# Performance work log

Measured on AMD Instinct MI355X. Metric: run time of the kernel, lower is better.

Reference implementation:

```python
import jax, jax.numpy as jnp
import numpy as np

N_ATOMS = 100000
N_BONDS = 200000
N_MOLS = 4000
ATOMS_PER_MOL = 25
MAX_NB = 6
ATOM_FDIM = 133
BOND_FDIM = 14
HIDDEN = 300
DEPTH = 3


def setup_inputs() -> dict:
    key = jax.random.key(0)
    ks = jax.random.split(key, 8)
    f_atoms = jax.random.normal(ks[0], (N_ATOMS, ATOM_FDIM), dtype=jnp.float32)
    f_bonds = jax.random.normal(ks[1], (N_BONDS, BOND_FDIM), dtype=jnp.float32)
    # incoming-bond lists per atom (irregular gather targets)
    a2b = jax.random.randint(ks[2], (N_ATOMS, MAX_NB), 0, N_BONDS, dtype=jnp.int32)
    # source atom of each directed bond
    b2a = jax.random.randint(ks[3], (N_BONDS,), 0, N_ATOMS, dtype=jnp.int32)
    # reverse bond: directed bonds come in pairs (2i, 2i+1)
    b2revb = (jnp.arange(N_BONDS, dtype=jnp.int32) ^ 1)
    # contiguous [start, size] per molecule
    starts = jnp.arange(N_MOLS, dtype=jnp.int32) * ATOMS_PER_MOL
    sizes = jnp.full((N_MOLS,), ATOMS_PER_MOL, dtype=jnp.int32)
    a_scope = jnp.stack([starts, sizes], axis=1)
    W_i = jax.random.normal(ks[4], (HIDDEN, ATOM_FDIM + BOND_FDIM), dtype=jnp.float32) * 0.05
    W_h = jax.random.normal(ks[5], (HIDDEN, HIDDEN), dtype=jnp.float32) * 0.05
    W_o = jax.random.normal(ks[6], (HIDDEN, ATOM_FDIM + HIDDEN), dtype=jnp.float32) * 0.05
    b_o = jax.random.normal(ks[7], (HIDDEN,), dtype=jnp.float32) * 0.05
    return {"f_atoms": f_atoms, "f_bonds": f_bonds, "a2b": a2b, "b2a": b2a,
            "b2revb": b2revb, "a_scope": a_scope, "W_i": W_i, "W_h": W_h,
            "W_o": W_o, "b_o": b_o}


def reference(f_atoms, f_bonds, a2b, b2a, b2revb, a_scope, W_i, W_h, W_o, b_o):
    # initial directed-bond messages: [f_atoms[src], f_bonds] -> Linear -> ReLU
    input_feats = jnp.concatenate([f_atoms[b2a], f_bonds], axis=1)  # (E, 147)
    message = jax.nn.relu(input_feats @ W_i.T)  # (E, H)
    for _ in range(DEPTH - 1):
        nei_a_message = message[a2b].sum(axis=1)          # (V, H) gather+sum
        nei_message = nei_a_message[b2a] - message[b2revb]  # (E, H)
        message = jax.nn.relu(nei_message @ W_h.T)
    a_message = message[a2b].sum(axis=1)  # (V, H)
    atom_hiddens = jax.nn.relu(jnp.concatenate([f_atoms, a_message], axis=1) @ W_o.T + b_o)
    # vectorized scope mean-pool (scopes are contiguous ranges)
    starts = a_scope[:, 0]
    sizes = a_scope[:, 1]
    seg_ids = jnp.searchsorted(starts, jnp.arange(atom_hiddens.shape[0]), side='right') - 1
    sums = jax.ops.segment_sum(atom_hiddens, seg_ids, num_segments=N_MOLS)
    denom = jnp.maximum(sizes, 1).astype(atom_hiddens.dtype)[:, None]
    mol_vecs = jnp.where((sizes > 0)[:, None], sums / denom, 0.0)
    return mol_vecs
```

## Files before the change

kernel.cpp:

```cpp
#include <hip/hip_runtime.h>
#include <stdint.h>

#define N_ATOMS   100000
#define N_BONDS   200000
#define N_MOLS    4000
#define MAX_NB    6
#define ATOM_FDIM 133
#define BOND_FDIM 14
#define HIDDEN    300
#define NPAD      320

typedef __attribute__((ext_vector_type(8))) short          bf16x8;
typedef __attribute__((ext_vector_type(8))) unsigned short u16x8;
typedef __attribute__((ext_vector_type(4))) float          f32x4;
typedef __attribute__((ext_vector_type(4))) unsigned int   u32x4;

static __device__ __forceinline__ float u2f(unsigned int u) {
  union { unsigned int u; float f; } v; v.u = u; return v.f;
}
static __device__ __forceinline__ unsigned int f2u(float f) {
  union { float f; unsigned int u; } v; v.f = f; return v.u;
}
static __device__ __forceinline__ float bflo(unsigned int u) { return u2f(u << 16); }
static __device__ __forceinline__ float bfhi(unsigned int u) { return u2f(u & 0xffff0000u); }
static __device__ __forceinline__ unsigned short f2bf_rn(float f) {
  unsigned int u = f2u(f);
  return (unsigned short)((u + 0x7fffu + ((u >> 16) & 1u)) >> 16);
}
static __device__ __forceinline__ unsigned int pack_rn(float lo, float hi) {
  return ((unsigned int)f2bf_rn(hi) << 16) | f2bf_rn(lo);
}

__global__ __launch_bounds__(256) void convin_kernel(
    const float* __restrict__ w, unsigned short* __restrict__ o, int N, int K, int KP) {
  size_t total = (size_t)N * KP;
  for (size_t idx = (size_t)blockIdx.x * 256 + threadIdx.x; idx < total; idx += (size_t)gridDim.x * 256) {
    int n = (int)(idx / KP), k = (int)(idx - (size_t)n * KP);
    float v = (k < K) ? w[(size_t)n * K + k] : 0.f;
    o[idx] = f2bf_rn(v);
  }
}

__global__ __launch_bounds__(256) void convw_kernel(
    const float* __restrict__ w, unsigned short* __restrict__ o,
    int Ksrc, int seg1, int src2off, int seg2dst, int seg2len, int KP) {
  int total = NPAD * KP;
  for (int idx = blockIdx.x * 256 + threadIdx.x; idx < total; idx += gridDim.x * 256) {
    int n = idx / KP, k = idx - n * KP;
    int src = -1;
    if (k < seg1) src = k;
    else if (k >= seg2dst && k < seg2dst + seg2len) src = src2off + (k - seg2dst);
    float v = (n < HIDDEN && src >= 0) ? w[(size_t)n * Ksrc + src] : 0.f;
    o[idx] = f2bf_rn(v);
  }
}

template<int KP, int SEG, bool RELU>
__global__ __launch_bounds__(256) void gemm_tp(
    const unsigned short* S1, const unsigned short* __restrict__ S2,
    const int* __restrict__ gmap, const unsigned short* __restrict__ W,
    unsigned short* out, int M, int nTiles) {
  constexpr int CHUNKS = KP / 8;
  constexpr int NST    = KP / 32;
  __shared__ __align__(16) unsigned short As[2 * 64 * KP];

  const int tid  = threadIdx.x;
  const int lane = tid & 63;
  const int wv   = tid >> 6;
  const int ar   = lane & 15, kq = lane >> 4;
  const int nbase = wv * 80;
  const unsigned short* Wl = W + (size_t)(nbase + ar) * KP + kq * 8;

  auto rowof = [&](int tile) { int r = tile * 64 + lane; return (r < M) ? r : (M - 1); };

  auto stage = [&](int buf, int drow, int srow) {
    char* base = (char*)As + (size_t)buf * (64 * KP * 2);
#pragma unroll
    for (int cs = wv; cs < CHUNKS; cs += 4) {
      const unsigned short* src;
      if (SEG == 0) src = S1 + (size_t)drow * KP + cs * 8;
      else src = (cs < 20) ? (S1 + (size_t)srow * 160 + cs * 8)
                           : (S2 + (size_t)drow * 32 + (cs - 20) * 8);
      __builtin_amdgcn_global_load_lds(
          (const __attribute__((address_space(1))) void*)src,
          (__attribute__((address_space(3))) void*)(base + (size_t)cs * 1024), 16, 0, 0);
    }
  };

  f32x4 acc[4][5];

  auto compute = [&](int buf) {
    const char* base = (const char*)As + (size_t)buf * (64 * KP * 2);
    bf16x8 bnxt[5];
#pragma unroll
    for (int nf = 0; nf < 5; nf++) bnxt[nf] = *(const bf16x8*)(Wl + (size_t)nf * 16 * KP);
#pragma unroll
    for (int ks = 0; ks < NST; ks++) {
      bf16x8 bcur[5];
#pragma unroll
      for (int nf = 0; nf < 5; nf++) bcur[nf] = bnxt[nf];
      if (ks + 1 < NST) {
#pragma unroll
        for (int nf = 0; nf < 5; nf++)
          bnxt[nf] = *(const bf16x8*)(Wl + (size_t)nf * 16 * KP + (ks + 1) * 32);
      }
      bf16x8 af[4];
#pragma unroll
      for (int m = 0; m < 4; m++)
        af[m] = *(const bf16x8*)(base + (size_t)((ks * 4 + kq) * 64 + m * 16 + ar) * 16);
#pragma unroll
      for (int nf = 0; nf < 5; nf++)
#pragma unroll
        for (int m = 0; m < 4; m++)
          acc[m][nf] = __builtin_amdgcn_mfma_f32_16x16x32_bf16(af[m], bcur[nf], acc[m][nf], 0, 0, 0);
    }
  };

  auto storeC = [&](int tile) {
#pragma unroll
    for (int m = 0; m < 4; m++)
#pragma unroll
      for (int rr = 0; rr < 4; rr++) {
        int orow = tile * 64 + m * 16 + kq * 4 + rr;
        if (orow >= M) continue;
#pragma unroll
        for (int nf = 0; nf < 5; nf++) {
          float v = acc[m][nf][rr];
          if (RELU) v = v > 0.f ? v : 0.f;
          out[(size_t)orow * NPAD + nbase + nf * 16 + ar] = f2bf_rn(v);
        }
      }
  };

  int t = blockIdx.x;
  if (t >= nTiles) return;
  {
    int srow0 = (SEG == 1) ? gmap[rowof(t)] : 0;
    stage(0, rowof(t), srow0);
  }
  int tn = t + gridDim.x;
  int g_n = (SEG == 1 && tn < nTiles) ? gmap[rowof(tn)] : 0;
  __syncthreads();

  int cur = 0;
  while (t < nTiles) {
    const int nxt = t + gridDim.x;
    if (nxt < nTiles) stage(cur ^ 1, rowof(nxt), g_n);
    const int t2 = nxt + gridDim.x;
    int g_n2 = (SEG == 1 && t2 < nTiles) ? gmap[rowof(t2)] : 0;
#pragma unroll
    for (int m = 0; m < 4; m++)
#pragma unroll
      for (int n = 0; n < 5; n++) acc[m][n] = (f32x4){0.f, 0.f, 0.f, 0.f};
    compute(cur);
    __syncthreads();
    storeC(t);
    cur ^= 1; t = nxt; g_n = g_n2;
  }
}

__global__ __launch_bounds__(256) void gemm_tpf(
    const unsigned short* Z, const unsigned short* __restrict__ Nei,
    const int* __restrict__ b2a, const unsigned short* __restrict__ W,
    unsigned short* out, int nTiles) {
  constexpr int KP = 320, BK = 160, NCH = 2, NSTC = 5, NREG = 5;
  __shared__ __align__(16) unsigned short As[2 * 64 * BK];

  const int tid  = threadIdx.x;
  const int lane = tid & 63;
  const int wv   = tid >> 6;
  const int ar   = lane & 15, kq = lane >> 4;
  const int nbase = wv * 80;
  const unsigned short* Wl = W + (size_t)(nbase + ar) * KP + kq * 8;

  u32x4 nei4[NREG], z4[NREG];

  auto loadreg = [&](int tile, int chunk) {
    const int row = tile * 64 + lane;
    const int g   = b2a[row];
    const int rev = row ^ 1;
    const int kb  = chunk * BK;
#pragma unroll
    for (int i = 0; i < NREG; i++) {
      const int cs = i * 4 + wv;
      nei4[i] = *(const u32x4*)(Nei + (size_t)g * NPAD + kb + cs * 8);
      z4[i]   = *(const u32x4*)(Z + (size_t)rev * NPAD + kb + cs * 8);
    }
  };

  auto writestage = [&](int buf) {
    char* base = (char*)As + (size_t)buf * (64 * BK * 2);
#pragma unroll
    for (int i = 0; i < NREG; i++) {
      const int cs = i * 4 + wv;
      u32x4 o;
#pragma unroll
      for (int t4 = 0; t4 < 4; t4++) {
        float lo = bflo(nei4[i][t4]) - bflo(z4[i][t4]);
        float hi = bfhi(nei4[i][t4]) - bfhi(z4[i][t4]);
        lo = lo > 0.f ? lo : 0.f; hi = hi > 0.f ? hi : 0.f;
        o[t4] = pack_rn(lo, hi);
      }
      *(u32x4*)(base + (size_t)(cs * 64 + lane) * 16) = o;
    }
  };

  f32x4 acc[4][5];

  auto compute = [&](int buf, int chunk) {
    const char* base = (const char*)As + (size_t)buf * (64 * BK * 2);
    const int kb = chunk * BK;
#pragma unroll
    for (int ks = 0; ks < NSTC; ks++) {
      bf16x8 af[4];
#pragma unroll
      for (int m = 0; m < 4; m++)
        af[m] = *(const bf16x8*)(base + (size_t)((ks * 4 + kq) * 64 + m * 16 + ar) * 16);
#pragma unroll
      for (int nf = 0; nf < 5; nf++) {
        bf16x8 bfr = *(const bf16x8*)(Wl + (size_t)nf * 16 * KP + kb + ks * 32);
#pragma unroll
        for (int m = 0; m < 4; m++)
          acc[m][nf] = __builtin_amdgcn_mfma_f32_16x16x32_bf16(af[m], bfr, acc[m][nf], 0, 0, 0);
      }
    }
  };

  auto storeC = [&](int tile) {
#pragma unroll
    for (int m = 0; m < 4; m++)
#pragma unroll
      for (int rr = 0; rr < 4; rr++) {
        int orow = tile * 64 + m * 16 + kq * 4 + rr;
#pragma unroll
        for (int nf = 0; nf < 5; nf++)
          out[(size_t)orow * NPAD + nbase + nf * 16 + ar] = f2bf_rn(acc[m][nf][rr]);
      }
  };

  int t = blockIdx.x;
  if (t >= nTiles) return;
  loadreg(t, 0);
  writestage(0);
  __syncthreads();

  int cur = 0;
  while (t < nTiles) {
#pragma unroll
    for (int m = 0; m < 4; m++)
#pragma unroll
      for (int n = 0; n < 5; n++) acc[m][n] = (f32x4){0.f, 0.f, 0.f, 0.f};
#pragma unroll
    for (int c = 0; c < NCH; c++) {
      int nt = t, nc = c + 1;
      if (nc == NCH) { nt = t + gridDim.x; nc = 0; }
      const bool valid = nt < nTiles;
      if (valid) loadreg(nt, nc);
      compute(cur, c);
      if (valid) writestage(cur ^ 1);
      __syncthreads();
      cur ^= 1;
    }
    storeC(t);
    t += gridDim.x;
  }
}

__global__ __launch_bounds__(256, 2) void gemm_bpo(
    const float* __restrict__ Af, const unsigned short* Ab,
    const unsigned short* __restrict__ W, const float* __restrict__ bias,
    unsigned short* out, int M) {
  constexpr int KP = 480, NST = 15;
  __shared__ __align__(16) unsigned short As[NST * 2048];

  const int b0   = blockIdx.x * 64;
  const int tid  = threadIdx.x;
  const int lane = tid & 63;
  const int wave = tid >> 6;
  const int sr   = tid >> 2;
  const int q    = tid & 3;

  int row = b0 + sr;
  if (row >= M) row = M - 1;
  const int dbase = (sr >> 4) * 512 + (q * 16 + (sr & 15)) * 8;

  auto stage_chunk = [&](int ks) -> u16x8 {
    const int kc = ks * 32 + q * 8;
    u16x8 r;
    if (kc >= 160) {
      r = *(const u16x8*)(Ab + (size_t)row * NPAD + (kc - 160));
    } else {
#pragma unroll
      for (int j = 0; j < 8; j++) {
        int k = kc + j;
        r[j] = (k < ATOM_FDIM) ? f2bf_rn(Af[(size_t)row * ATOM_FDIM + k]) : (unsigned short)0;
      }
    }
    return r;
  };

  constexpr int G = 5;
#pragma unroll
  for (int ks0 = 0; ks0 < NST; ks0 += G) {
    u16x8 vals[G];
#pragma unroll
    for (int j = 0; j < G; j++) { int ks = ks0 + j; if (ks < NST) vals[j] = stage_chunk(ks); }
#pragma unroll
    for (int j = 0; j < G; j++) { int ks = ks0 + j; if (ks < NST) *(u16x8*)&As[ks * 2048 + dbase] = vals[j]; }
  }
  __syncthreads();

  f32x4 acc[4][5];
#pragma unroll
  for (int m = 0; m < 4; m++)
#pragma unroll
    for (int n = 0; n < 5; n++) acc[m][n] = (f32x4){0.f, 0.f, 0.f, 0.f};

  const int nbase = wave * 80;
  const int ar = lane & 15, kq = lane >> 4;
  const unsigned short* Wl = W + (size_t)(nbase + ar) * KP + kq * 8;

  bf16x8 bnxt[5];
#pragma unroll
  for (int nf = 0; nf < 5; nf++) bnxt[nf] = *(const bf16x8*)(Wl + (size_t)nf * 16 * KP);

#pragma unroll
  for (int ks = 0; ks < NST; ks++) {
    bf16x8 bcur[5];
#pragma unroll
    for (int nf = 0; nf < 5; nf++) bcur[nf] = bnxt[nf];
    if (ks + 1 < NST) {
#pragma unroll
      for (int nf = 0; nf < 5; nf++)
        bnxt[nf] = *(const bf16x8*)(Wl + (size_t)nf * 16 * KP + (ks + 1) * 32);
    }
    bf16x8 af[4];
#pragma unroll
    for (int m = 0; m < 4; m++) af[m] = *(const bf16x8*)&As[ks * 2048 + m * 512 + lane * 8];
#pragma unroll
    for (int nf = 0; nf < 5; nf++)
#pragma unroll
      for (int m = 0; m < 4; m++)
        acc[m][nf] = __builtin_amdgcn_mfma_f32_16x16x32_bf16(af[m], bcur[nf], acc[m][nf], 0, 0, 0);
  }

#pragma unroll
  for (int m = 0; m < 4; m++) {
#pragma unroll
    for (int rr = 0; rr < 4; rr++) {
      int orow = b0 + m * 16 + kq * 4 + rr;
      if (orow >= M) continue;
#pragma unroll
      for (int nf = 0; nf < 5; nf++) {
        int ocol = nbase + nf * 16 + ar;
        float v = acc[m][nf][rr];
        v += (ocol < HIDDEN) ? bias[ocol] : 0.f;
        v = v > 0.f ? v : 0.f;
        out[(size_t)orow * NPAD + ocol] = f2bf_rn(v);
      }
    }
  }
}

__global__ __launch_bounds__(256) void agg_kernel(
    const unsigned short* __restrict__ src, const int* __restrict__ a2b,
    unsigned short* __restrict__ dst) {
  const int TPA = NPAD / 16;
  int idx = blockIdx.x * 256 + threadIdx.x;
  if (idx >= N_ATOMS * TPA) return;
  int a  = idx / TPA;
  int kc = (idx - a * TPA) * 16;
  int bidx[MAX_NB];
#pragma unroll
  for (int j = 0; j < MAX_NB; j++) bidx[j] = a2b[a * MAX_NB + j];
  float slo[8], shi[8];
#pragma unroll
  for (int t = 0; t < 8; t++) { slo[t] = 0.f; shi[t] = 0.f; }
#pragma unroll
  for (int j = 0; j < MAX_NB; j++) {
    const u32x4* p = (const u32x4*)(src + (size_t)bidx[j] * NPAD + kc);
    u32x4 v0 = p[0], v1 = p[1];
#pragma unroll
    for (int t = 0; t < 4; t++) {
      slo[t]     += bflo(v0[t]); shi[t]     += bfhi(v0[t]);
      slo[4 + t] += bflo(v1[t]); shi[4 + t] += bfhi(v1[t]);
    }
  }
  u32x4 o0, o1;
#pragma unroll
  for (int t = 0; t < 4; t++) { o0[t] = pack_rn(slo[t], shi[t]); o1[t] = pack_rn(slo[4 + t], shi[4 + t]); }
  u32x4* qp = (u32x4*)(dst + (size_t)a * NPAD + kc);
  qp[0] = o0; qp[1] = o1;
}

__global__ __launch_bounds__(256) void combineH_kernel(
    const unsigned short* __restrict__ neiZ, const unsigned short* Zh,
    const int* __restrict__ b2a, unsigned short* msg) {
  const int TPB = NPAD / 16;
  const int NPAIR = N_BONDS / 2;
  int idx = blockIdx.x * 256 + threadIdx.x;
  if (idx >= NPAIR * TPB) return;
  int p  = idx / TPB;
  int kc = (idx - p * TPB) * 16;
  int b0i = 2 * p, b1i = 2 * p + 1;
  int g0 = b2a[b0i], g1 = b2a[b1i];
  const u32x4* pn0 = (const u32x4*)(neiZ + (size_t)g0 * NPAD + kc);
  const u32x4* pn1 = (const u32x4*)(neiZ + (size_t)g1 * NPAD + kc);
  const u32x4* pz0 = (const u32x4*)(Zh + (size_t)b1i * NPAD + kc);
  const u32x4* pz1 = (const u32x4*)(Zh + (size_t)b0i * NPAD + kc);
  u32x4 n00 = pn0[0], n01 = pn0[1], n10 = pn1[0], n11 = pn1[1];
  u32x4 z00 = pz0[0], z01 = pz0[1], z10 = pz1[0], z11 = pz1[1];
  u32x4 o00, o01, o10, o11;
#pragma unroll
  for (int t = 0; t < 4; t++) {
    float a, c;
    a = bflo(n00[t]) - bflo(z00[t]); c = bfhi(n00[t]) - bfhi(z00[t]);
    o00[t] = pack_rn(a > 0.f ? a : 0.f, c > 0.f ? c : 0.f);
    a = bflo(n01[t]) - bflo(z01[t]); c = bfhi(n01[t]) - bfhi(z01[t]);
    o01[t] = pack_rn(a > 0.f ? a : 0.f, c > 0.f ? c : 0.f);
    a = bflo(n10[t]) - bflo(z10[t]); c = bfhi(n10[t]) - bfhi(z10[t]);
    o10[t] = pack_rn(a > 0.f ? a : 0.f, c > 0.f ? c : 0.f);
    a = bflo(n11[t]) - bflo(z11[t]); c = bfhi(n11[t]) - bfhi(z11[t]);
    o11[t] = pack_rn(a > 0.f ? a : 0.f, c > 0.f ? c : 0.f);
  }
  u32x4* q0 = (u32x4*)(msg + (size_t)b0i * NPAD + kc);
  u32x4* q1 = (u32x4*)(msg + (size_t)b1i * NPAD + kc);
  q0[0] = o00; q0[1] = o01; q1[0] = o10; q1[1] = o11;
}

__global__ __launch_bounds__(256) void readout_kernel(
    const unsigned short* __restrict__ hidden, const int* __restrict__ a_scope,
    float* __restrict__ out) {
  const int TPM = NPAD / 8;
  int idx = blockIdx.x * 256 + threadIdx.x;
  if (idx >= N_MOLS * TPM) return;
  int m = idx / TPM;
  int c = (idx - m * TPM) * 8;
  int start = a_scope[m * 2], size = a_scope[m * 2 + 1];
  float s[8];
#pragma unroll
  for (int t = 0; t < 8; t++) s[t] = 0.f;
  for (int i = 0; i < size; i++) {
    const u32x4 v = *(const u32x4*)(hidden + (size_t)(start + i) * NPAD + c);
#pragma unroll
    for (int t = 0; t < 4; t++) { s[2 * t] += bflo(v[t]); s[2 * t + 1] += bfhi(v[t]); }
  }
  float inv = (size > 0) ? 1.f / (float)size : 0.f;
#pragma unroll
  for (int t = 0; t < 8; t++) {
    int col = c + t;
    if (col < HIDDEN) out[(size_t)m * HIDDEN + col] = s[t] * inv;
  }
}

extern "C" void kernel_launch(void* const* d_in, const int* in_sizes, int n_in,
                              void* d_out, int out_size, void* d_ws, size_t ws_size,
                              hipStream_t stream) {
  const float* f_atoms = (const float*)d_in[0];
  const float* f_bonds = (const float*)d_in[1];
  const int*   a2b     = (const int*)d_in[2];
  const int*   b2a     = (const int*)d_in[3];
  const int*   a_scope = (const int*)d_in[5];
  const float* W_i     = (const float*)d_in[6];
  const float* W_h     = (const float*)d_in[7];
  const float* W_o     = (const float*)d_in[8];
  const float* b_o     = (const float*)d_in[9];
  float* out = (float*)d_out;

  char* ws = (char*)d_ws;
  size_t off = 0;
  auto alloc = [&](size_t bytes) { size_t o = off; off += (bytes + 255) & ~(size_t)255; return o; };
  unsigned short* P     = (unsigned short*)(ws + alloc((size_t)N_BONDS * NPAD * 2));
  unsigned short* R     = (unsigned short*)(ws + alloc((size_t)N_ATOMS * NPAD * 2));
  unsigned short* fa_bf = (unsigned short*)(ws + alloc((size_t)N_ATOMS * 160 * 2));
  unsigned short* fb_bf = (unsigned short*)(ws + alloc((size_t)N_BONDS * 32 * 2));
  unsigned short* WiAB  = (unsigned short*)(ws + alloc((size_t)NPAD * 192 * 2));
  unsigned short* Wh    = (unsigned short*)(ws + alloc((size_t)NPAD * 320 * 2));
  unsigned short* Wo    = (unsigned short*)(ws + alloc((size_t)NPAD * 480 * 2));

  convin_kernel<<<2048, 256, 0, stream>>>(f_atoms, fa_bf, N_ATOMS, ATOM_FDIM, 160);
  convin_kernel<<<2048, 256, 0, stream>>>(f_bonds, fb_bf, N_BONDS, BOND_FDIM, 32);
  convw_kernel<<<(NPAD * 192 + 255) / 256, 256, 0, stream>>>(W_i, WiAB, 147, 133, 133, 160, 14, 192);
  convw_kernel<<<(NPAD * 320 + 255) / 256, 256, 0, stream>>>(W_h, Wh, 300, 300, 0, 0, 0, 320);
  convw_kernel<<<(NPAD * 480 + 255) / 256, 256, 0, stream>>>(W_o, Wo, 433, 133, 133, 160, 300, 480);

  const int nTilesB = N_BONDS / 64;
  const int gridA = (N_ATOMS + 63) / 64;
  const int gagg = (N_ATOMS * (NPAD / 16) + 255) / 256;
  const int gpar = ((N_BONDS / 2) * (NPAD / 16) + 255) / 256;

  gemm_tp<192, 1, true><<<768, 256, 0, stream>>>(
      fa_bf, fb_bf, b2a, WiAB, P, N_BONDS, nTilesB);

  gemm_tp<320, 0, false><<<512, 256, 0, stream>>>(
      P, nullptr, nullptr, Wh, P, N_BONDS, nTilesB);
  agg_kernel<<<gagg, 256, 0, stream>>>(P, a2b, R);

  gemm_tpf<<<512, 256, 0, stream>>>(P, R, b2a, Wh, P, nTilesB);

  agg_kernel<<<gagg, 256, 0, stream>>>(P, a2b, R);
  combineH_kernel<<<gpar, 256, 0, stream>>>(R, P, b2a, P);

  agg_kernel<<<gagg, 256, 0, stream>>>(P, a2b, R);
  gemm_bpo<<<gridA, 256, 0, stream>>>(f_atoms, R, Wo, b_o, R, N_ATOMS);

  readout_kernel<<<(N_MOLS * (NPAD / 8) + 255) / 256, 256, 0, stream>>>(R, a_scope, out);
}
```

Measured before the change: 641.7 us.

## Make output GEMM persistent and double-buffered with async global-to-LDS loads

Replaces the one-tile-per-block output GEMM with a persistent kernel on 512 blocks. It streams the concatenated [atom features, aggregated messages] operand into double-buffered LDS chunks using global_load_lds, so loads for the next chunk overlap MFMA work on the current one. It reads the pre-converted bf16 atom features instead of converting fp32 inputs on the fly. W fragments are now loaded per k-step without register prefetch, and the kernel no longer uses the 2-blocks-per-CU launch bound, which may change occupancy.

```diff
diff --git a/kernel.cpp b/kernel.cpp
--- a/kernel.cpp
+++ b/kernel.cpp
@@ -266,99 +266,96 @@
   }
 }
 
-__global__ __launch_bounds__(256, 2) void gemm_bpo(
-    const float* __restrict__ Af, const unsigned short* Ab,
+__global__ __launch_bounds__(256) void gemm_tpo(
+    const unsigned short* __restrict__ fa_bf, const unsigned short* Ab,
     const unsigned short* __restrict__ W, const float* __restrict__ bias,
-    unsigned short* out, int M) {
-  constexpr int KP = 480, NST = 15;
-  __shared__ __align__(16) unsigned short As[NST * 2048];
-
-  const int b0   = blockIdx.x * 64;
+    unsigned short* out, int M, int nTiles) {
+  constexpr int KP = 480, BK = 160, NCH = 3, NSTC = 5, CHG = 20;
+  __shared__ __align__(16) unsigned short As[2 * 64 * BK];
+
   const int tid  = threadIdx.x;
   const int lane = tid & 63;
-  const int wave = tid >> 6;
-  const int sr   = tid >> 2;
-  const int q    = tid & 3;
-
-  int row = b0 + sr;
-  if (row >= M) row = M - 1;
-  const int dbase = (sr >> 4) * 512 + (q * 16 + (sr & 15)) * 8;
-
-  auto stage_chunk = [&](int ks) -> u16x8 {
-    const int kc = ks * 32 + q * 8;
-    u16x8 r;
-    if (kc >= 160) {
-      r = *(const u16x8*)(Ab + (size_t)row * NPAD + (kc - 160));
-    } else {
-#pragma unroll
-      for (int j = 0; j < 8; j++) {
-        int k = kc + j;
-        r[j] = (k < ATOM_FDIM) ? f2bf_rn(Af[(size_t)row * ATOM_FDIM + k]) : (unsigned short)0;
-      }
-    }
-    return r;
-  };
-
-  constexpr int G = 5;
-#pragma unroll
-  for (int ks0 = 0; ks0 < NST; ks0 += G) {
-    u16x8 vals[G];
-#pragma unroll
-    for (int j = 0; j < G; j++) { int ks = ks0 + j; if (ks < NST) vals[j] = stage_chunk(ks); }
-#pragma unroll
-    for (int j = 0; j < G; j++) { int ks = ks0 + j; if (ks < NST) *(u16x8*)&As[ks * 2048 + dbase] = vals[j]; }
-  }
+  const int wv   = tid >> 6;
+  const int ar   = lane & 15, kq = lane >> 4;
+  const int nbase = wv * 80;
+  const unsigned short* Wl = W + (size_t)(nbase + ar) * KP + kq * 8;
+
+  auto stage = [&](int buf, int tile, int chunk) {
+    char* base = (char*)As + (size_t)buf * (64 * BK * 2);
+    int r = tile * 64 + lane; if (r >= M) r = M - 1;
+#pragma unroll
+    for (int cl = wv; cl < CHG; cl += 4) {
+      const int ae = (chunk * CHG + cl) * 8;
+      const unsigned short* src = (ae < 160)
+          ? (fa_bf + (size_t)r * 160 + ae)
+          : (Ab + (size_t)r * NPAD + (ae - 160));
+      __builtin_amdgcn_global_load_lds(
+          (const __attribute__((address_space(1))) void*)src,
+          (__attribute__((address_space(3))) void*)(base + (size_t)cl * 1024), 16, 0, 0);
+    }
+  };
+
+  f32x4 acc[4][5];
+
+  auto compute = [&](int buf, int chunk) {
+    const char* base = (const char*)As + (size_t)buf * (64 * BK * 2);
+    const int kb = chunk * BK;
+#pragma unroll
+    for (int ks = 0; ks < NSTC; ks++) {
+      bf16x8 af[4];
+#pragma unroll
+      for (int m = 0; m < 4; m++)
+        af[m] = *(const bf16x8*)(base + (size_t)((ks * 4 + kq) * 64 + m * 16 + ar) * 16);
+#pragma unroll
+      for (int nf = 0; nf < 5; nf++) {
+        bf16x8 bfr = *(const bf16x8*)(Wl + (size_t)nf * 16 * KP + kb + ks * 32);
+#pragma unroll
+        for (int m = 0; m < 4; m++)
+          acc[m][nf] = __builtin_amdgcn_mfma_f32_16x16x32_bf16(af[m], bfr, acc[m][nf], 0, 0, 0);
+      }
+    }
+  };
+
+  auto storeC = [&](int tile) {
+#pragma unroll
+    for (int m = 0; m < 4; m++)
+#pragma unroll
+      for (int rr = 0; rr < 4; rr++) {
+        int orow = tile * 64 + m * 16 + kq * 4 + rr;
+        if (orow >= M) continue;
+#pragma unroll
+        for (int nf = 0; nf < 5; nf++) {
+          int ocol = nbase + nf * 16 + ar;
+          float v = acc[m][nf][rr];
+          v += (ocol < HIDDEN) ? bias[ocol] : 0.f;
+          v = v > 0.f ? v : 0.f;
+          out[(size_t)orow * NPAD + ocol] = f2bf_rn(v);
+        }
+      }
+  };
+
+  int t = blockIdx.x;
+  if (t >= nTiles) return;
+  stage(0, t, 0);
   __syncthreads();
 
-  f32x4 acc[4][5];
-#pragma unroll
-  for (int m = 0; m < 4; m++)
-#pragma unroll
-    for (int n = 0; n < 5; n++) acc[m][n] = (f32x4){0.f, 0.f, 0.f, 0.f};
-
-  const int nbase = wave * 80;
-  const int ar = lane & 15, kq = lane >> 4;
-  const unsigned short* Wl = W + (size_t)(nbase + ar) * KP + kq * 8;
-
-  bf16x8 bnxt[5];
-#pragma unroll
-  for (int nf = 0; nf < 5; nf++) bnxt[nf] = *(const bf16x8*)(Wl + (size_t)nf * 16 * KP);
-
-#pragma unroll
-  for (int ks = 0; ks < NST; ks++) {
-    bf16x8 bcur[5];
-#pragma unroll
-    for (int nf = 0; nf < 5; nf++) bcur[nf] = bnxt[nf];
-    if (ks + 1 < NST) {
-#pragma unroll
-      for (int nf = 0; nf < 5; nf++)
-        bnxt[nf] = *(const bf16x8*)(Wl + (size_t)nf * 16 * KP + (ks + 1) * 32);
-    }
-    bf16x8 af[4];
-#pragma unroll
-    for (int m = 0; m < 4; m++) af[m] = *(const bf16x8*)&As[ks * 2048 + m * 512 + lane * 8];
-#pragma unroll
-    for (int nf = 0; nf < 5; nf++)
-#pragma unroll
-      for (int m = 0; m < 4; m++)
-        acc[m][nf] = __builtin_amdgcn_mfma_f32_16x16x32_bf16(af[m], bcur[nf], acc[m][nf], 0, 0, 0);
-  }
-
-#pragma unroll
-  for (int m = 0; m < 4; m++) {
-#pragma unroll
-    for (int rr = 0; rr < 4; rr++) {
-      int orow = b0 + m * 16 + kq * 4 + rr;
-      if (orow >= M) continue;
-#pragma unroll
-      for (int nf = 0; nf < 5; nf++) {
-        int ocol = nbase + nf * 16 + ar;
-        float v = acc[m][nf][rr];
-        v += (ocol < HIDDEN) ? bias[ocol] : 0.f;
-        v = v > 0.f ? v : 0.f;
-        out[(size_t)orow * NPAD + ocol] = f2bf_rn(v);
-      }
-    }
+  int cur = 0;
+  while (t < nTiles) {
+#pragma unroll
+    for (int m = 0; m < 4; m++)
+#pragma unroll
+      for (int n = 0; n < 5; n++) acc[m][n] = (f32x4){0.f, 0.f, 0.f, 0.f};
+#pragma unroll
+    for (int c = 0; c < NCH; c++) {
+      int nt = t, nc = c + 1;
+      if (nc == NCH) { nt = t + gridDim.x; nc = 0; }
+      if (nt < nTiles) stage(cur ^ 1, nt, nc);
+      compute(cur, c);
+      __syncthreads();
+      cur ^= 1;
+    }
+    storeC(t);
+    t += gridDim.x;
   }
 }
 
@@ -485,7 +482,7 @@
   convw_kernel<<<(NPAD * 480 + 255) / 256, 256, 0, stream>>>(W_o, Wo, 433, 133, 133, 160, 300, 480);
 
   const int nTilesB = N_BONDS / 64;
-  const int gridA = (N_ATOMS + 63) / 64;
+  const int nTilesA = (N_ATOMS + 63) / 64;
   const int gagg = (N_ATOMS * (NPAD / 16) + 255) / 256;
   const int gpar = ((N_BONDS / 2) * (NPAD / 16) + 255) / 256;
 
@@ -502,7 +499,7 @@
   combineH_kernel<<<gpar, 256, 0, stream>>>(R, P, b2a, P);
 
   agg_kernel<<<gagg, 256, 0, stream>>>(P, a2b, R);
-  gemm_bpo<<<gridA, 256, 0, stream>>>(f_atoms, R, Wo, b_o, R, N_ATOMS);
+  gemm_tpo<<<512, 256, 0, stream>>>(fa_bf, R, Wo, b_o, R, N_ATOMS, nTilesA);
 
   readout_kernel<<<(N_MOLS * (NPAD / 8) + 255) / 256, 256, 0, stream>>>(R, a_scope, out);
 }
```

Measured after the change: 640.9 us, median of 3. About the same (-0.1%).
